# Kernel optimization log

Hardware: AMD Instinct MI355X
Metric: run time of the kernel (lower is better)

## Reference

```python
import jax, jax.numpy as jnp
import numpy as np

T, D = 8192, 1024      # num flattened tokens, hidden_dim
E, K = 8, 2            # n_experts, num_experts_per_tok


def setup_inputs() -> dict:
    key = jax.random.key(0)
    k1, k2, k3, k4, k5 = jax.random.split(key, 5)
    x = jax.random.normal(k1, (T, D), dtype=jnp.float32)
    flat_expert_indices = jax.random.randint(k2, (T * K,), 0, E, dtype=jnp.int32)
    flat_expert_weights = jax.random.uniform(k3, (T * K,), dtype=jnp.float32)
    # Expert params: fc1/fc2 are bias-free Linears, stored torch-style [out, in]
    W1 = jax.random.normal(k4, (E, D, D), dtype=jnp.float32) * (1.0 / np.sqrt(D))
    W2 = jax.random.normal(k5, (E, D, D), dtype=jnp.float32) * (1.0 / np.sqrt(D))
    return {"x": x, "flat_expert_indices": flat_expert_indices,
            "flat_expert_weights": flat_expert_weights, "W1": W1, "W2": W2}


def reference(x, flat_expert_indices, flat_expert_weights, W1, W2):
    # DummyExpert: relu(relu(x @ W1.T) @ W2.T), per expert (torch Linear = x @ W.T)
    # Dense dispatch: compute every expert on every token, then gather the
    # top-k expert outputs per token and combine with routing weights.
    h = jax.nn.relu(jnp.einsum('td,eod->eto', x, W1))   # [E, T, D]
    y = jax.nn.relu(jnp.einsum('eto,epo->etp', h, W2))  # [E, T, D]
    idx = flat_expert_indices.reshape(T, K)             # [T, K]
    w = flat_expert_weights.reshape(T, K)               # [T, K]
    yt = jnp.transpose(y, (1, 0, 2))                    # [T, E, D]
    sel = jnp.take_along_axis(yt, idx[:, :, None].astype(jnp.int32), axis=1)  # [T, K, D]
    return jnp.sum(sel * w[:, :, None], axis=1)         # [T, D]
```

## Files before the change

kernel.cpp:

```cpp
#include <hip/hip_runtime.h>

typedef unsigned short u16;
typedef unsigned int   u32;
typedef unsigned long long u64;
typedef __attribute__((ext_vector_type(8))) short short8;
typedef __attribute__((ext_vector_type(4))) float f32x4;

#define T_TOK 8192
#define DIM   1024
#define NEXP  8
#define NPAIR (T_TOK * 2)
#define MAXTILES 136

__device__ __forceinline__ u16 f2bf(float f) {
  u32 u = __builtin_bit_cast(u32, f);
  u32 r = (u + 0x7fffu + ((u >> 16) & 1u)) >> 16;
  return (u16)r;
}
__device__ __forceinline__ float bf2f(u16 b) {
  return __builtin_bit_cast(float, ((u32)b) << 16);
}

__device__ __forceinline__ void gl_lds16(const u16* g, u16* l) {
  __builtin_amdgcn_global_load_lds(
      (const __attribute__((address_space(1))) u32*)g,
      (__attribute__((address_space(3))) u32*)l,
      16, 0, 0);
}

__global__ void cast3_k(const float* __restrict__ x, const float* __restrict__ W1,
                        const float* __restrict__ W2,
                        u16* __restrict__ xb, u16* __restrict__ w1b, u16* __restrict__ w2b) {
  const int g = (blockIdx.x * 256 + threadIdx.x) * 8;
  const int region = g >> 23;
  const int i = g & 0x7fffff;
  const float* s = (region == 0) ? x : (region == 1) ? W1 : W2;
  u16* d = (region == 0) ? xb : (region == 1) ? w1b : w2b;
  f32x4 a = *(const f32x4*)(s + i);
  f32x4 b = *(const f32x4*)(s + i + 4);
  short8 o;
  o[0] = (short)f2bf(a[0]); o[1] = (short)f2bf(a[1]);
  o[2] = (short)f2bf(a[2]); o[3] = (short)f2bf(a[3]);
  o[4] = (short)f2bf(b[0]); o[5] = (short)f2bf(b[1]);
  o[6] = (short)f2bf(b[2]); o[7] = (short)f2bf(b[3]);
  *(short8*)(d + i) = o;
}

__global__ void sort_pairs_k(const int* __restrict__ idx,
                             int* __restrict__ counts, int* __restrict__ offsets,
                             int* __restrict__ bucket, int* __restrict__ pos,
                             int* __restrict__ tlist, int* __restrict__ ntiles) {
  __shared__ int lc[16][NEXP];
  __shared__ int lo[16][NEXP];
  const int tid  = threadIdx.x;
  const int w    = tid >> 6;
  const int lane = tid & 63;
  const u64 ltmask = (lane == 63) ? 0x7fffffffffffffffull : ((1ull << lane) - 1);

  int e_i[16];
#pragma unroll
  for (int i = 0; i < 16; ++i) e_i[i] = idx[(w * 16 + i) * 64 + lane];

  int cnt[NEXP] = {};
#pragma unroll
  for (int i = 0; i < 16; ++i) {
#pragma unroll
    for (int ex = 0; ex < NEXP; ++ex) {
      u64 m = __ballot(e_i[i] == ex);
      cnt[ex] += (int)__popcll(m);
    }
  }
  if (lane == 0) {
#pragma unroll
    for (int ex = 0; ex < NEXP; ++ex) lc[w][ex] = cnt[ex];
  }
  __syncthreads();

  if (tid == 0) {
    int s = 0;
    int c8[NEXP];
    for (int ex = 0; ex < NEXP; ++ex) {
      offsets[ex] = s;
      int c = 0;
      for (int ww = 0; ww < 16; ++ww) { lo[ww][ex] = s; s += lc[ww][ex]; c += lc[ww][ex]; }
      counts[ex] = c;
      c8[ex] = c;
    }
    int t = 0;
    for (int r = 0; r < 128; ++r)
      for (int ex = 0; ex < NEXP; ++ex)
        if (r * 128 < c8[ex]) tlist[t++] = (r << 3) | ex;
    *ntiles = t;
  }
  __syncthreads();

  int cur[NEXP];
#pragma unroll
  for (int ex = 0; ex < NEXP; ++ex) cur[ex] = lo[w][ex];
#pragma unroll
  for (int i = 0; i < 16; ++i) {
    const int item = (w * 16 + i) * 64 + lane;
    const int e = e_i[i];
    int p = 0;
#pragma unroll
    for (int ex = 0; ex < NEXP; ++ex) {
      u64 m = __ballot(e == ex);
      int rank = (int)__popcll(m & ltmask);
      if (e == ex) p = cur[ex] + rank;
      cur[ex] += (int)__popcll(m);
    }
    bucket[p] = item;
    pos[item] = p;
  }
}

template <int GATHER>
__global__ __launch_bounds__(256, 3)
void moe_gemm_k(const u16* __restrict__ A,
                const u16* __restrict__ W,
                u16* __restrict__ O,
                const int* __restrict__ counts,
                const int* __restrict__ offsets,
                const int* __restrict__ bucket,
                const int* __restrict__ tlist,
                const int* __restrict__ ntiles) {
  if ((int)blockIdx.x >= *ntiles) return;
  const int info = tlist[blockIdx.x];
  const int e    = info & 7;
  const int m0   = (info >> 3) << 7;
  const int cnt  = counts[e];
  const int seg  = offsets[e];
  const int n0   = blockIdx.y << 7;

  __shared__ u16 As[128 * 64];
  __shared__ u16 Bs[128 * 64];

  const int tid  = threadIdx.x;
  const int lane = tid & 63;
  const int wave = tid >> 6;

  int aoff[4], boff[4];
#pragma unroll
  for (int j = 0; j < 4; ++j) {
    const int c   = ((wave << 2) + j) * 64 + lane;
    const int r   = c >> 3;
    const int c16 = (c & 7) ^ (r & 7);
    int p = seg + m0 + r;
    p = (p < seg + cnt) ? p : (seg + cnt - 1);
    int rowbase;
    if (GATHER) { const int pair = bucket[p]; rowbase = (pair >> 1) * DIM; }
    else        { rowbase = p * DIM; }
    aoff[j] = rowbase + (c16 << 3);
    boff[j] = e * DIM * DIM + (n0 + r) * DIM + (c16 << 3);
  }

  f32x4 acc[4][4] = {};

  const int wm   = (wave >> 1) << 6;
  const int wn   = (wave & 1) << 6;
  const int lr   = lane & 15;
  const int quad = lane >> 4;

  for (int k0 = 0; k0 < DIM; k0 += 64) {
    __syncthreads();
#pragma unroll
    for (int j = 0; j < 4; ++j) {
      const int instr = (wave << 2) + j;
      gl_lds16(A + aoff[j] + k0, &As[instr << 9]);
      gl_lds16(W + boff[j] + k0, &Bs[instr << 9]);
    }
    __syncthreads();

#pragma unroll
    for (int kk = 0; kk < 64; kk += 32) {
      const int qb = (kk >> 3) + quad;
      short8 af[4], bf[4];
#pragma unroll
      for (int mi = 0; mi < 4; ++mi) {
        const int r = wm + (mi << 4) + lr;
        af[mi] = *(const short8*)&As[r * 64 + ((qb ^ (r & 7)) << 3)];
      }
#pragma unroll
      for (int ni = 0; ni < 4; ++ni) {
        const int r = wn + (ni << 4) + lr;
        bf[ni] = *(const short8*)&Bs[r * 64 + ((qb ^ (r & 7)) << 3)];
      }
#pragma unroll
      for (int mi = 0; mi < 4; ++mi)
#pragma unroll
        for (int ni = 0; ni < 4; ++ni)
          acc[mi][ni] = __builtin_amdgcn_mfma_f32_16x16x32_bf16(af[mi], bf[ni], acc[mi][ni], 0, 0, 0);
    }
  }

  const int pend = seg + cnt;
#pragma unroll
  for (int mi = 0; mi < 4; ++mi) {
#pragma unroll
    for (int ni = 0; ni < 4; ++ni) {
      const int col = n0 + wn + (ni << 4) + lr;
#pragma unroll
      for (int r4 = 0; r4 < 4; ++r4) {
        const int p = seg + m0 + wm + (mi << 4) + (quad << 2) + r4;
        if (p < pend) {
          float v = acc[mi][ni][r4];
          v = v > 0.f ? v : 0.f;
          O[(size_t)p * DIM + col] = f2bf(v);
        }
      }
    }
  }
}

__global__ void combine_k(const u16* __restrict__ y, const int* __restrict__ pos,
                          const float* __restrict__ wts, float* __restrict__ out) {
  const int t    = blockIdx.x * 2 + (threadIdx.x >> 7);
  const int lane = threadIdx.x & 127;
  const int col  = lane * 8;
  const int p0 = pos[2 * t], p1 = pos[2 * t + 1];
  const float w0 = wts[2 * t], w1 = wts[2 * t + 1];
  const short8 a = *(const short8*)(y + (size_t)p0 * DIM + col);
  const short8 b = *(const short8*)(y + (size_t)p1 * DIM + col);
  f32x4 o0, o1;
#pragma unroll
  for (int j = 0; j < 8; ++j) {
    float v = w0 * bf2f((u16)a[j]) + w1 * bf2f((u16)b[j]);
    if (j < 4) o0[j] = v; else o1[j - 4] = v;
  }
  float* op = out + (size_t)t * DIM + col;
  *(f32x4*)op = o0;
  *(f32x4*)(op + 4) = o1;
}

extern "C" void kernel_launch(void* const* d_in, const int* in_sizes, int n_in,
                              void* d_out, int out_size, void* d_ws, size_t ws_size,
                              hipStream_t stream) {
  const float* x   = (const float*)d_in[0];
  const int*   idx = (const int*)d_in[1];
  const float* wts = (const float*)d_in[2];
  const float* W1  = (const float*)d_in[3];
  const float* W2  = (const float*)d_in[4];
  float* out = (float*)d_out;

  char* ws = (char*)d_ws;
  int* counts  = (int*)ws;
  int* offsets = (int*)(ws + 32);
  int* ntiles  = (int*)(ws + 64);
  int* tlist   = (int*)(ws + 128);
  int* bucket  = (int*)(ws + 1024);
  int* pos     = (int*)(ws + 1024 + 4 * NPAIR);
  const size_t base = 132096;
  const size_t MB16 = 16ull * 1024 * 1024;
  u16* xb  = (u16*)(ws + base);
  u16* w1b = (u16*)(ws + base + MB16);
  u16* w2b = (u16*)(ws + base + 2 * MB16);
  u16* h   = (u16*)(ws + base + 3 * MB16);
  u16* yb  = xb;

  cast3_k<<<3 * 4096, 256, 0, stream>>>(x, W1, W2, xb, w1b, w2b);
  sort_pairs_k<<<1, 1024, 0, stream>>>(idx, counts, offsets, bucket, pos, tlist, ntiles);

  dim3 gg(MAXTILES, DIM / 128);
  moe_gemm_k<1><<<gg, 256, 0, stream>>>(xb, w1b, h, counts, offsets, bucket, tlist, ntiles);
  moe_gemm_k<0><<<gg, 256, 0, stream>>>(h, w2b, yb, counts, offsets, bucket, tlist, ntiles);

  combine_k<<<T_TOK / 2, 256, 0, stream>>>(yb, pos, wts, out);
}
```

Before: 275.5 us.

## Fuse cast with routing sort and enlarge GEMM M-tile to 256 rows

Merges the bf16 cast kernel and the single-block routing sort into one launch, with the last block doing the sort using 4 waves instead of 16. Doubles the grouped GEMM M-tile to 256 rows with 512-thread blocks, so each weight tile loaded into LDS is reused across twice as many tokens and fewer tiles are launched. The sort block now does more serial work per wave and may finish late. Larger tiles waste more padding rows per expert and lower the number of blocks per CU.

```diff
diff --git a/kernel.cpp b/kernel.cpp
--- a/kernel.cpp
+++ b/kernel.cpp
@@ -10,7 +10,8 @@
 #define DIM   1024
 #define NEXP  8
 #define NPAIR (T_TOK * 2)
-#define MAXTILES 136
+#define MAXTILES 72
+#define NCASTBLK 12288
 
 __device__ __forceinline__ u16 f2bf(float f) {
   u32 u = __builtin_bit_cast(u32, f);
@@ -28,45 +29,43 @@
       16, 0, 0);
 }
 
-__global__ void cast3_k(const float* __restrict__ x, const float* __restrict__ W1,
-                        const float* __restrict__ W2,
-                        u16* __restrict__ xb, u16* __restrict__ w1b, u16* __restrict__ w2b) {
-  const int g = (blockIdx.x * 256 + threadIdx.x) * 8;
-  const int region = g >> 23;
-  const int i = g & 0x7fffff;
-  const float* s = (region == 0) ? x : (region == 1) ? W1 : W2;
-  u16* d = (region == 0) ? xb : (region == 1) ? w1b : w2b;
-  f32x4 a = *(const f32x4*)(s + i);
-  f32x4 b = *(const f32x4*)(s + i + 4);
-  short8 o;
-  o[0] = (short)f2bf(a[0]); o[1] = (short)f2bf(a[1]);
-  o[2] = (short)f2bf(a[2]); o[3] = (short)f2bf(a[3]);
-  o[4] = (short)f2bf(b[0]); o[5] = (short)f2bf(b[1]);
-  o[6] = (short)f2bf(b[2]); o[7] = (short)f2bf(b[3]);
-  *(short8*)(d + i) = o;
-}
-
-__global__ void sort_pairs_k(const int* __restrict__ idx,
-                             int* __restrict__ counts, int* __restrict__ offsets,
-                             int* __restrict__ bucket, int* __restrict__ pos,
-                             int* __restrict__ tlist, int* __restrict__ ntiles) {
-  __shared__ int lc[16][NEXP];
-  __shared__ int lo[16][NEXP];
+__global__ void cast_sort_k(const float* __restrict__ x, const float* __restrict__ W1,
+                            const float* __restrict__ W2,
+                            u16* __restrict__ xb, u16* __restrict__ w1b, u16* __restrict__ w2b,
+                            const int* __restrict__ idx,
+                            int* __restrict__ counts, int* __restrict__ offsets,
+                            int* __restrict__ bucket, int* __restrict__ pos,
+                            int* __restrict__ tlist, int* __restrict__ ntiles) {
+  if (blockIdx.x < NCASTBLK) {
+    const int g = (blockIdx.x * 256 + threadIdx.x) * 8;
+    const int region = g >> 23;
+    const int i = g & 0x7fffff;
+    const float* s = (region == 0) ? x : (region == 1) ? W1 : W2;
+    u16* d = (region == 0) ? xb : (region == 1) ? w1b : w2b;
+    f32x4 a = *(const f32x4*)(s + i);
+    f32x4 b = *(const f32x4*)(s + i + 4);
+    short8 o;
+    o[0] = (short)f2bf(a[0]); o[1] = (short)f2bf(a[1]);
+    o[2] = (short)f2bf(a[2]); o[3] = (short)f2bf(a[3]);
+    o[4] = (short)f2bf(b[0]); o[5] = (short)f2bf(b[1]);
+    o[6] = (short)f2bf(b[2]); o[7] = (short)f2bf(b[3]);
+    *(short8*)(d + i) = o;
+    return;
+  }
+
+  __shared__ int lc[4][NEXP];
+  __shared__ int lo[4][NEXP];
   const int tid  = threadIdx.x;
   const int w    = tid >> 6;
   const int lane = tid & 63;
   const u64 ltmask = (lane == 63) ? 0x7fffffffffffffffull : ((1ull << lane) - 1);
 
-  int e_i[16];
-#pragma unroll
-  for (int i = 0; i < 16; ++i) e_i[i] = idx[(w * 16 + i) * 64 + lane];
-
   int cnt[NEXP] = {};
-#pragma unroll
-  for (int i = 0; i < 16; ++i) {
+  for (int i = 0; i < 64; ++i) {
+    const int e = idx[w * 4096 + i * 64 + lane];
 #pragma unroll
     for (int ex = 0; ex < NEXP; ++ex) {
-      u64 m = __ballot(e_i[i] == ex);
+      u64 m = __ballot(e == ex);
       cnt[ex] += (int)__popcll(m);
     }
   }
@@ -82,14 +81,14 @@
     for (int ex = 0; ex < NEXP; ++ex) {
       offsets[ex] = s;
       int c = 0;
-      for (int ww = 0; ww < 16; ++ww) { lo[ww][ex] = s; s += lc[ww][ex]; c += lc[ww][ex]; }
+      for (int ww = 0; ww < 4; ++ww) { lo[ww][ex] = s; s += lc[ww][ex]; c += lc[ww][ex]; }
       counts[ex] = c;
       c8[ex] = c;
     }
     int t = 0;
-    for (int r = 0; r < 128; ++r)
+    for (int r = 0; r < 64; ++r)
       for (int ex = 0; ex < NEXP; ++ex)
-        if (r * 128 < c8[ex]) tlist[t++] = (r << 3) | ex;
+        if (r * 256 < c8[ex]) tlist[t++] = (r << 3) | ex;
     *ntiles = t;
   }
   __syncthreads();
@@ -97,10 +96,9 @@
   int cur[NEXP];
 #pragma unroll
   for (int ex = 0; ex < NEXP; ++ex) cur[ex] = lo[w][ex];
-#pragma unroll
-  for (int i = 0; i < 16; ++i) {
-    const int item = (w * 16 + i) * 64 + lane;
-    const int e = e_i[i];
+  for (int i = 0; i < 64; ++i) {
+    const int item = w * 4096 + i * 64 + lane;
+    const int e = idx[item];
     int p = 0;
 #pragma unroll
     for (int ex = 0; ex < NEXP; ++ex) {
@@ -115,7 +113,7 @@
 }
 
 template <int GATHER>
-__global__ __launch_bounds__(256, 3)
+__global__ __launch_bounds__(512, 4)
 void moe_gemm_k(const u16* __restrict__ A,
                 const u16* __restrict__ W,
                 u16* __restrict__ O,
@@ -127,19 +125,19 @@
   if ((int)blockIdx.x >= *ntiles) return;
   const int info = tlist[blockIdx.x];
   const int e    = info & 7;
-  const int m0   = (info >> 3) << 7;
+  const int m0   = (info >> 3) << 8;
   const int cnt  = counts[e];
   const int seg  = offsets[e];
   const int n0   = blockIdx.y << 7;
 
-  __shared__ u16 As[128 * 64];
+  __shared__ u16 As[256 * 64];
   __shared__ u16 Bs[128 * 64];
 
   const int tid  = threadIdx.x;
   const int lane = tid & 63;
   const int wave = tid >> 6;
 
-  int aoff[4], boff[4];
+  int aoff[4], boff[2];
 #pragma unroll
   for (int j = 0; j < 4; ++j) {
     const int c   = ((wave << 2) + j) * 64 + lane;
@@ -151,6 +149,12 @@
     if (GATHER) { const int pair = bucket[p]; rowbase = (pair >> 1) * DIM; }
     else        { rowbase = p * DIM; }
     aoff[j] = rowbase + (c16 << 3);
+  }
+#pragma unroll
+  for (int j = 0; j < 2; ++j) {
+    const int c   = ((wave << 1) + j) * 64 + lane;
+    const int r   = c >> 3;
+    const int c16 = (c & 7) ^ (r & 7);
     boff[j] = e * DIM * DIM + (n0 + r) * DIM + (c16 << 3);
   }
 
@@ -164,11 +168,11 @@
   for (int k0 = 0; k0 < DIM; k0 += 64) {
     __syncthreads();
 #pragma unroll
-    for (int j = 0; j < 4; ++j) {
-      const int instr = (wave << 2) + j;
-      gl_lds16(A + aoff[j] + k0, &As[instr << 9]);
-      gl_lds16(W + boff[j] + k0, &Bs[instr << 9]);
-    }
+    for (int j = 0; j < 4; ++j)
+      gl_lds16(A + aoff[j] + k0, &As[((wave << 2) + j) << 9]);
+#pragma unroll
+    for (int j = 0; j < 2; ++j)
+      gl_lds16(W + boff[j] + k0, &Bs[((wave << 1) + j) << 9]);
     __syncthreads();
 
 #pragma unroll
@@ -257,12 +261,13 @@
   u16* h   = (u16*)(ws + base + 3 * MB16);
   u16* yb  = xb;
 
-  cast3_k<<<3 * 4096, 256, 0, stream>>>(x, W1, W2, xb, w1b, w2b);
-  sort_pairs_k<<<1, 1024, 0, stream>>>(idx, counts, offsets, bucket, pos, tlist, ntiles);
+  cast_sort_k<<<NCASTBLK + 1, 256, 0, stream>>>(x, W1, W2, xb, w1b, w2b,
+                                                idx, counts, offsets, bucket, pos,
+                                                tlist, ntiles);
 
   dim3 gg(MAXTILES, DIM / 128);
-  moe_gemm_k<1><<<gg, 256, 0, stream>>>(xb, w1b, h, counts, offsets, bucket, tlist, ntiles);
-  moe_gemm_k<0><<<gg, 256, 0, stream>>>(h, w2b, yb, counts, offsets, bucket, tlist, ntiles);
+  moe_gemm_k<1><<<gg, 512, 0, stream>>>(xb, w1b, h, counts, offsets, bucket, tlist, ntiles);
+  moe_gemm_k<0><<<gg, 512, 0, stream>>>(h, w2b, yb, counts, offsets, bucket, tlist, ntiles);
 
   combine_k<<<T_TOK / 2, 256, 0, stream>>>(yb, pos, wts, out);
 }
```

After: 302.2 us. 9.7% more time.
